# Kernel optimization log

Measured on AMD Instinct MI355X. Metric: run time of the kernel, lower is better.

Reference implementation:

```python
import jax, jax.numpy as jnp
import numpy as np

N_NODES = 100000
N_EDGES = 1280000
D_IN = 64
D_HID = 64


def _sage_conv(x, src, dst, deg, Wl, bl, Wr):
    # gather source-node features per edge, scatter-mean to destination nodes
    msg = x[src]                                            # [E, d]
    agg = jax.ops.segment_sum(msg, dst, num_segments=N_NODES)  # [N, d]
    mean = agg / deg                                        # [N, d]
    # PyG SAGEConv: lin_l(aggregated) + lin_r(root); bias lives in lin_l
    return mean @ Wl.T + bl + x @ Wr.T


def setup_inputs() -> dict:
    key = jax.random.key(0)
    ks = jax.random.split(key, 10)
    x = jax.random.normal(ks[0], (N_NODES, D_IN), dtype=jnp.float32)
    edge_index = jax.random.randint(ks[1], (2, N_EDGES), 0, N_NODES, dtype=jnp.int64)
    s = 1.0 / np.sqrt(D_IN)
    W1l = jax.random.uniform(ks[2], (D_HID, D_IN), jnp.float32, -s, s)
    W1r = jax.random.uniform(ks[3], (D_HID, D_IN), jnp.float32, -s, s)
    b1 = jax.random.uniform(ks[4], (D_HID,), jnp.float32, -s, s)
    s2 = 1.0 / np.sqrt(D_HID)
    W2l = jax.random.uniform(ks[5], (D_HID, D_HID), jnp.float32, -s2, s2)
    W2r = jax.random.uniform(ks[6], (D_HID, D_HID), jnp.float32, -s2, s2)
    b2 = jax.random.uniform(ks[7], (D_HID,), jnp.float32, -s2, s2)
    Wh = jax.random.uniform(ks[8], (1, D_HID), jnp.float32, -s2, s2)
    bh = jax.random.uniform(ks[9], (1,), jnp.float32, -s2, s2)
    return {"x": x, "edge_index": edge_index, "W1l": W1l, "W1r": W1r, "b1": b1,
            "W2l": W2l, "W2r": W2r, "b2": b2, "Wh": Wh, "bh": bh}


def reference(x, edge_index, W1l, W1r, b1, W2l, W2r, b2, Wh, bh):
    src, dst = edge_index[0], edge_index[1]
    # in-degree for mean aggregation (clamped to avoid div-by-zero)
    deg = jax.ops.segment_sum(jnp.ones((N_EDGES,), jnp.float32), dst,
                              num_segments=N_NODES)
    deg = jnp.maximum(deg, 1.0)[:, None]                    # [N, 1]
    h = jax.nn.relu(_sage_conv(x, src, dst, deg, W1l, b1, W1r))
    h = jax.nn.relu(_sage_conv(h, src, dst, deg, W2l, b2, W2r))
    out = (h @ Wh.T + bh)[:, 0]                             # [N]
    return out, h
```

## Files before the change

kernel.cpp:

```cpp
#include <hip/hip_runtime.h>

#define N_NODES 100000
#define N_EDGES 1280000
#define D 64
#define NPAD 102400
#define CAP 48
#define NBUCK 391
#define AB 313
#define NT16 6250
#define XQ (N_NODES * 16)
#define CVTOT (XQ + 32 + 4096)
#define SPLIT 720000
#define CV1 384
#define CV2 384

typedef __attribute__((ext_vector_type(8))) short bf16x8;
typedef __attribute__((ext_vector_type(4))) float f32x4;
typedef __attribute__((ext_vector_type(2))) float f32x2;

__device__ __forceinline__ unsigned short f2bf(float f) {
    union { float f; unsigned u; } c; c.f = f;
    unsigned u = c.u;
    return (unsigned short)((u + 0x7FFF + ((u >> 16) & 1)) >> 16);
}
__device__ __forceinline__ float fp8d(unsigned b) {
    unsigned t = ((b & 0x80u) << 24) | ((b & 0x7fu) << 20);
    union { unsigned u; float f; } c; c.u = t;
    return c.f * 1.32922799578491587e36f;
}
__device__ __forceinline__ unsigned char f2fp8(float f) {
    f = fminf(fmaxf(f, -448.f), 448.f);
    float g = f * 7.52316384526264005e-37f;
    union { float f; unsigned u; } c; c.f = g;
    unsigned gb = c.u;
    unsigned r = (((gb & 0x7fffffffu) + 0x7ffffu + ((gb >> 20) & 1u)) >> 20) & 0x7fu;
    return (unsigned char)(((gb >> 24) & 0x80u) | r);
}

__device__ __forceinline__ void cvt_range(
    int gtid, int gsz, int lo0, int hi,
    const float* __restrict__ x,
    const float* __restrict__ W1l, const float* __restrict__ W1r,
    const float* __restrict__ W2l, const float* __restrict__ W2r,
    unsigned short* __restrict__ xb, unsigned short* __restrict__ h1b,
    unsigned char* __restrict__ x8, unsigned char* __restrict__ h8,
    unsigned short* __restrict__ wb)
{
    for (int i = lo0 + gtid; i < hi; i += gsz) {
        if (i < XQ) {
            float4 v = ((const float4*)x)[i];
            ((ushort4*)xb)[i] = make_ushort4(f2bf(v.x), f2bf(v.y), f2bf(v.z), f2bf(v.w));
            ((uchar4*)x8)[i]  = make_uchar4(f2fp8(v.x), f2fp8(v.y), f2fp8(v.z), f2fp8(v.w));
        } else if (i < XQ + 32) {
            int k = i - XQ;
            if (k < 16) {
                ((ushort4*)xb)[(size_t)N_NODES * 16 + k] = make_ushort4(0,0,0,0);
                ((unsigned*)x8)[(size_t)N_NODES * 16 + k] = 0u;
            } else {
                ((ushort4*)h1b)[(size_t)N_NODES * 16 + (k - 16)] = make_ushort4(0,0,0,0);
                ((unsigned*)h8)[(size_t)N_NODES * 16 + (k - 16)] = 0u;
            }
        } else {
            int wf = i - XQ - 32;
            int m = wf >> 10, k = wf & 1023;
            const float* s = (m == 0) ? W1l : (m == 1) ? W1r : (m == 2) ? W2l : W2r;
            float4 v = ((const float4*)s)[k];
            ((ushort4*)wb)[m * 1024 + k] =
                make_ushort4(f2bf(v.x), f2bf(v.y), f2bf(v.z), f2bf(v.w));
        }
    }
}

__global__ __launch_bounds__(512) void prep_kernel(
    const float* __restrict__ x,
    const int* __restrict__ src, const int* __restrict__ dst,
    const float* __restrict__ W1l, const float* __restrict__ W1r,
    const float* __restrict__ W2l, const float* __restrict__ W2r,
    unsigned short* __restrict__ xb, unsigned short* __restrict__ h1b,
    unsigned char* __restrict__ x8, unsigned char* __restrict__ h8,
    unsigned short* __restrict__ wb,
    int* __restrict__ sorted, int* __restrict__ exclT)
{
    __shared__ int cntA[392];
    __shared__ int excl[392];
    __shared__ int stage_pk[4096];

    const int t   = threadIdx.x;
    const int bid = blockIdx.x;

    if (bid < AB) {
        const int e0 = bid * 4096;
        const int cbatch = min(4096, N_EDGES - e0);

        if (t < 392) cntA[t] = 0;
        __syncthreads();

        int mb[8], mr[8], mpk[8];
#pragma unroll
        for (int i = 0; i < 8; ++i) {
            int idx = i * 512 + t;
            mb[i] = -1;
            if (idx < cbatch) {
                int e = e0 + idx;
                int s = src[e], d = dst[e];
                int b = d >> 8;
                mb[i]  = b;
                mpk[i] = (s << 8) | (d & 255);
                mr[i]  = atomicAdd(&cntA[b], 1);
            }
        }
        __syncthreads();

        if (t < 64) {
            int pre[7], tot = 0;
            if (t < 56) {
#pragma unroll
                for (int i = 0; i < 7; ++i) { pre[i] = tot; tot += cntA[t * 7 + i]; }
            }
            int sc = tot;
#pragma unroll
            for (int off = 1; off < 64; off <<= 1) {
                int u = __shfl_up(sc, off, 64);
                if (t >= off) sc += u;
            }
            int ex = sc - tot;
            if (t < 56) {
#pragma unroll
                for (int i = 0; i < 7; ++i) excl[t * 7 + i] = ex + pre[i];
            }
        }
        __syncthreads();

#pragma unroll
        for (int i = 0; i < 8; ++i) {
            if (mb[i] >= 0)
                stage_pk[excl[mb[i]] + mr[i]] = mpk[i];
        }
        __syncthreads();

#pragma unroll
        for (int i = 0; i < 8; ++i) {
            int idx = i * 512 + t;
            if (idx < cbatch) sorted[e0 + idx] = stage_pk[idx];
        }
        if (t < 392) exclT[bid * 392 + t] = excl[t];
    } else {
        const int gtid = (bid - AB) * 512 + t;
        cvt_range(gtid, CV1 * 512, 0, SPLIT,
                  x, W1l, W1r, W2l, W2r, xb, h1b, x8, h8, wb);
    }
}

__global__ __launch_bounds__(512) void binB_kernel(
    const int* __restrict__ sorted, const int* __restrict__ exclT,
    int* __restrict__ csr, int* __restrict__ deg,
    const float* __restrict__ x,
    const float* __restrict__ W1l, const float* __restrict__ W1r,
    const float* __restrict__ W2l, const float* __restrict__ W2r,
    unsigned short* __restrict__ xb, unsigned short* __restrict__ h1b,
    unsigned char* __restrict__ x8, unsigned char* __restrict__ h8,
    unsigned short* __restrict__ wb)
{
    __shared__ int cur[256];
    __shared__ __align__(16) int lcsr[256 * CAP];

    const int t = threadIdx.x;
    const int k = blockIdx.x;

    if (k < NBUCK) {
        if (t < 256) cur[t] = 0;
        __syncthreads();

        for (int u = t; u < 2 * AB; u += 512) {
            int seg = u >> 1, half = u & 1;
            int s0  = exclT[seg * 392 + k];
            int cnt = exclT[seg * 392 + k + 1] - s0;
            int b0 = half ? (cnt >> 1) : 0;
            int b1 = half ? cnt : (cnt >> 1);
            const int* sp = sorted + seg * 4096 + s0 + b0;
            int m = b1 - b0;
            if (m > 0) {
                int pk = sp[0];
                for (int e = 0; e < m; ++e) {
                    int nxt = (e + 1 < m) ? sp[e + 1] : 0;
                    int nl = pk & 255;
                    int r  = atomicAdd(&cur[nl], 1);
                    if (r < CAP) lcsr[nl * CAP + r] = pk >> 8;
                    pk = nxt;
                }
            }
        }
        __syncthreads();

        const int base = k * 256;
        for (int i = t; i < 4096; i += 512) {
            int r = i >> 4, cc = i & 15;
            if (cc < 12) {
                int lenr = min(cur[r], CAP);
                if (cc * 4 < lenr)
                    *(int4*)(csr + (size_t)(base + r) * CAP + cc * 4) =
                        *(const int4*)(lcsr + r * CAP + cc * 4);
            }
        }
        if (t < 256) deg[base + t] = cur[t];
    } else {
        const int gtid = (k - NBUCK) * 512 + t;
        cvt_range(gtid, CV2 * 512, SPLIT, CVTOT,
                  x, W1l, W1r, W2l, W2r, xb, h1b, x8, h8, wb);
    }
}

template <int LAYER>
__global__ __launch_bounds__(256) void layer_kernel(
    const int* __restrict__ csr, const int* __restrict__ deg_g,
    const unsigned char*  __restrict__ feat8,
    const unsigned short* __restrict__ root_b,
    const unsigned short* __restrict__ wl_b,
    const float* __restrict__ bl,
    const unsigned short* __restrict__ wr_b,
    unsigned short* __restrict__ hout_b,
    unsigned char*  __restrict__ hout8,
    float* __restrict__ hout_f,
    const float* __restrict__ Wh, const float* __restrict__ bh,
    float* __restrict__ out)
{
    __shared__ __align__(16) char lds[9472];
    unsigned short* sA = (unsigned short*)lds;
    unsigned short* sX = sA + 16 * 72;
    float* sH    = (float*)(lds + 4608);
    float* spart = (float*)(lds + 8960);

    const int tid = threadIdx.x;
    const int n0  = blockIdx.x * 16;

    const int jt = tid >> 6;
    const int l64 = tid & 63;
    const int rowl = l64 & 15, quad = l64 >> 4;
    const unsigned short* wlp = wl_b + (jt * 16 + rowl) * 64 + quad * 8;
    const unsigned short* wrp = wr_b + (jt * 16 + rowl) * 64 + quad * 8;
    bf16x8 b0 = *(const bf16x8*)(wlp);
    bf16x8 b1 = *(const bf16x8*)(wlp + 32);
    bf16x8 b2 = *(const bf16x8*)(wrp);
    bf16x8 b3 = *(const bf16x8*)(wrp + 32);
    float bj = bl[jt * 16 + rowl];

    {
        int row = tid >> 4, c4 = tid & 15;
        ushort4 x4 = ((const ushort4*)root_b)[(size_t)(n0 + row) * 16 + c4];
        *(ushort4*)(sX + row * 72 + c4 * 4) = x4;
    }

    {
        const uint2* fb2 = (const uint2*)feat8;
        const int g   = tid >> 4;
        const int l   = tid & 15;
        const int h   = l >> 3;
        const int lo  = l & 7;
        const int n   = n0 + g;
        const int* rp = csr + (size_t)n * CAP;
        const int dg  = deg_g[n];
        const int id0 = rp[l];
        const int len = (dg < CAP) ? dg : CAP;
        f32x2 a0 = {0.f, 0.f}, a1 = {0.f, 0.f}, a2 = {0.f, 0.f}, a3 = {0.f, 0.f};

#if __has_builtin(__builtin_amdgcn_cvt_pk_f32_fp8)
#define GCHUNK(IDEXPR)                                                       \
        {                                                                    \
            int id_ = (IDEXPR);                                              \
            uint2 w[8];                                                      \
            _Pragma("unroll")                                                \
            for (int i = 0; i < 8; ++i)                                      \
                w[i] = fb2[(__shfl(id_, 2 * i + h, 16) << 3) + lo];          \
            _Pragma("unroll")                                                \
            for (int i = 0; i < 8; ++i) {                                    \
                a0 += __builtin_amdgcn_cvt_pk_f32_fp8((int)w[i].x, false);   \
                a1 += __builtin_amdgcn_cvt_pk_f32_fp8((int)w[i].x, true);    \
                a2 += __builtin_amdgcn_cvt_pk_f32_fp8((int)w[i].y, false);   \
                a3 += __builtin_amdgcn_cvt_pk_f32_fp8((int)w[i].y, true);    \
            }                                                                \
        }
#else
#define GCHUNK(IDEXPR)                                                       \
        {                                                                    \
            int id_ = (IDEXPR);                                              \
            uint2 w[8];                                                      \
            _Pragma("unroll")                                                \
            for (int i = 0; i < 8; ++i)                                      \
                w[i] = fb2[(__shfl(id_, 2 * i + h, 16) << 3) + lo];          \
            _Pragma("unroll")                                                \
            for (int i = 0; i < 8; ++i) {                                    \
                f32x2 p0 = {fp8d(w[i].x & 255), fp8d((w[i].x >> 8) & 255)};  \
                f32x2 p1 = {fp8d((w[i].x >> 16) & 255), fp8d(w[i].x >> 24)}; \
                f32x2 p2 = {fp8d(w[i].y & 255), fp8d((w[i].y >> 8) & 255)};  \
                f32x2 p3 = {fp8d((w[i].y >> 16) & 255), fp8d(w[i].y >> 24)}; \
                a0 += p0; a1 += p1; a2 += p2; a3 += p3;                      \
            }                                                                \
        }
#endif

        GCHUNK((l < len) ? id0 : N_NODES);
        for (int cb = 16; cb < len; cb += 16) {
            int idxl = cb + l;
            GCHUNK((idxl < len) ? rp[idxl] : N_NODES);
        }
#undef GCHUNK

        a0.x += __shfl_xor(a0.x, 8); a0.y += __shfl_xor(a0.y, 8);
        a1.x += __shfl_xor(a1.x, 8); a1.y += __shfl_xor(a1.y, 8);
        a2.x += __shfl_xor(a2.x, 8); a2.y += __shfl_xor(a2.y, 8);
        a3.x += __shfl_xor(a3.x, 8); a3.y += __shfl_xor(a3.y, 8);
        float inv = 1.0f / fmaxf((float)dg, 1.0f);
        if (h == 0) {
            *(ushort4*)(sA + g * 72 + lo * 8) =
                make_ushort4(f2bf(a0.x * inv), f2bf(a0.y * inv),
                             f2bf(a1.x * inv), f2bf(a1.y * inv));
            *(ushort4*)(sA + g * 72 + lo * 8 + 4) =
                make_ushort4(f2bf(a2.x * inv), f2bf(a2.y * inv),
                             f2bf(a3.x * inv), f2bf(a3.y * inv));
        }
    }
    __syncthreads();

    const unsigned short* ap = sA + rowl * 72 + quad * 8;
    const unsigned short* xp = sX + rowl * 72 + quad * 8;
    bf16x8 am0 = *(const bf16x8*)(ap);
    bf16x8 am1 = *(const bf16x8*)(ap + 32);
    bf16x8 ax0 = *(const bf16x8*)(xp);
    bf16x8 ax1 = *(const bf16x8*)(xp + 32);

    f32x4 acc = {0.f, 0.f, 0.f, 0.f};
    acc = __builtin_amdgcn_mfma_f32_16x16x32_bf16(am0, b0, acc, 0, 0, 0);
    acc = __builtin_amdgcn_mfma_f32_16x16x32_bf16(am1, b1, acc, 0, 0, 0);
    acc = __builtin_amdgcn_mfma_f32_16x16x32_bf16(ax0, b2, acc, 0, 0, 0);
    acc = __builtin_amdgcn_mfma_f32_16x16x32_bf16(ax1, b3, acc, 0, 0, 0);

#pragma unroll
    for (int r = 0; r < 4; ++r) {
        int node = quad * 4 + r;
        sH[node * 68 + jt * 16 + rowl] = fmaxf(acc[r] + bj, 0.f);
    }
    __syncthreads();

    if (LAYER == 2 && tid < 128) {
        int node = tid >> 3, q = tid & 7;
        float p = 0.f;
#pragma unroll
        for (int c = 0; c < 2; ++c) {
            float4 hv = *(const float4*)(sH + node * 68 + q * 8 + c * 4);
            float4 wv = ((const float4*)Wh)[q * 2 + c];
            p += hv.x * wv.x + hv.y * wv.y + hv.z * wv.z + hv.w * wv.w;
        }
        spart[tid] = p;
    }

    {
        int row = tid >> 4, c4 = tid & 15;
        int n = n0 + row;
        const float* hp = sH + row * 68 + c4 * 4;
        if (LAYER == 1) {
            ((ushort4*)hout_b)[(size_t)n * 16 + c4] =
                make_ushort4(f2bf(hp[0]), f2bf(hp[1]), f2bf(hp[2]), f2bf(hp[3]));
            ((uchar4*)hout8)[(size_t)n * 16 + c4] =
                make_uchar4(f2fp8(hp[0]), f2fp8(hp[1]), f2fp8(hp[2]), f2fp8(hp[3]));
        } else {
            ((float4*)hout_f)[(size_t)n * 16 + c4] =
                make_float4(hp[0], hp[1], hp[2], hp[3]);
        }
    }

    if (LAYER == 2) {
        __syncthreads();
        if (tid < 16) {
            float s = bh[0];
#pragma unroll
            for (int q = 0; q < 8; ++q) s += spart[tid * 8 + q];
            out[n0 + tid] = s;
        }
    }
}

extern "C" void kernel_launch(void* const* d_in, const int* in_sizes, int n_in,
                              void* d_out, int out_size, void* d_ws, size_t ws_size,
                              hipStream_t stream) {
    const float* x   = (const float*)d_in[0];
    const int*   ei  = (const int*)d_in[1];
    const int*   src = ei;
    const int*   dst = ei + N_EDGES;
    const float* W1l = (const float*)d_in[2];
    const float* W1r = (const float*)d_in[3];
    const float* b1  = (const float*)d_in[4];
    const float* W2l = (const float*)d_in[5];
    const float* W2r = (const float*)d_in[6];
    const float* b2  = (const float*)d_in[7];
    const float* Wh  = (const float*)d_in[8];
    const float* bh  = (const float*)d_in[9];

    float* out   = (float*)d_out;
    float* h_out = out + N_NODES;

    int* wsi = (int*)d_ws;
    int* deg = wsi;
    int* csr = deg + NPAD;
    unsigned short* wb  = (unsigned short*)(csr + NBUCK * 256 * CAP);
    unsigned short* x_b = wb + 16384;
    unsigned short* h1b = x_b + (size_t)(N_NODES + 1) * D;
    unsigned char*  x8  = (unsigned char*)(h1b + (size_t)(N_NODES + 1) * D);
    unsigned char*  h8  = x8 + (size_t)(N_NODES + 1) * D;
    int* sorted = (int*)h1b;
    int* exclT  = sorted + AB * 4096;

    unsigned short* w1l_b = wb;
    unsigned short* w1r_b = wb + 4096;
    unsigned short* w2l_b = wb + 8192;
    unsigned short* w2r_b = wb + 12288;

    prep_kernel<<<AB + CV1, 512, 0, stream>>>(
        x, src, dst, W1l, W1r, W2l, W2r, x_b, h1b, x8, h8, wb, sorted, exclT);

    binB_kernel<<<NBUCK + CV2, 512, 0, stream>>>(
        sorted, exclT, csr, deg,
        x, W1l, W1r, W2l, W2r, x_b, h1b, x8, h8, wb);

    layer_kernel<1><<<NT16, 256, 0, stream>>>(
        csr, deg, x8, x_b, w1l_b, b1, w1r_b, h1b, h8, nullptr,
        nullptr, nullptr, nullptr);
    layer_kernel<2><<<NT16, 256, 0, stream>>>(
        csr, deg, h8, h1b, w2l_b, b2, w2r_b, nullptr, nullptr, h_out,
        Wh, bh, out);
}
```

Before: 166.2 us.

## Shrink layer blocks to 8 nodes with 128 threads, two output tiles per wave

```diff
diff --git a/kernel.cpp b/kernel.cpp
--- a/kernel.cpp
+++ b/kernel.cpp
@@ -7,7 +7,7 @@
 #define CAP 48
 #define NBUCK 391
 #define AB 313
-#define NT16 6250
+#define NT8 12500
 #define XQ (N_NODES * 16)
 #define CVTOT (XQ + 32 + 4096)
 #define SPLIT 720000
@@ -211,7 +211,7 @@
 }
 
 template <int LAYER>
-__global__ __launch_bounds__(256) void layer_kernel(
+__global__ __launch_bounds__(128) void layer_kernel(
     const int* __restrict__ csr, const int* __restrict__ deg_g,
     const unsigned char*  __restrict__ feat8,
     const unsigned short* __restrict__ root_b,
@@ -224,25 +224,26 @@
     const float* __restrict__ Wh, const float* __restrict__ bh,
     float* __restrict__ out)
 {
-    __shared__ __align__(16) char lds[9472];
+    __shared__ __align__(16) char lds[4736];
     unsigned short* sA = (unsigned short*)lds;
-    unsigned short* sX = sA + 16 * 72;
-    float* sH    = (float*)(lds + 4608);
-    float* spart = (float*)(lds + 8960);
+    unsigned short* sX = sA + 8 * 72;
+    float* sH    = (float*)(lds + 2304);
+    float* spart = (float*)(lds + 4480);
 
     const int tid = threadIdx.x;
-    const int n0  = blockIdx.x * 16;
-
-    const int jt = tid >> 6;
+    const int n0  = blockIdx.x * 8;
+    const int wv  = tid >> 6;
     const int l64 = tid & 63;
     const int rowl = l64 & 15, quad = l64 >> 4;
-    const unsigned short* wlp = wl_b + (jt * 16 + rowl) * 64 + quad * 8;
-    const unsigned short* wrp = wr_b + (jt * 16 + rowl) * 64 + quad * 8;
-    bf16x8 b0 = *(const bf16x8*)(wlp);
-    bf16x8 b1 = *(const bf16x8*)(wlp + 32);
-    bf16x8 b2 = *(const bf16x8*)(wrp);
-    bf16x8 b3 = *(const bf16x8*)(wrp + 32);
-    float bj = bl[jt * 16 + rowl];
+
+    const int jt0 = wv * 2;
+    const unsigned short* wlp0 = wl_b + (jt0 * 16 + rowl) * 64 + quad * 8;
+    const unsigned short* wrp0 = wr_b + (jt0 * 16 + rowl) * 64 + quad * 8;
+    bf16x8 c00 = *(const bf16x8*)(wlp0);
+    bf16x8 c01 = *(const bf16x8*)(wlp0 + 32);
+    bf16x8 c02 = *(const bf16x8*)(wrp0);
+    bf16x8 c03 = *(const bf16x8*)(wrp0 + 32);
+    float bj0 = bl[jt0 * 16 + rowl];
 
     {
         int row = tid >> 4, c4 = tid & 15;
@@ -321,34 +322,52 @@
     }
     __syncthreads();
 
-    const unsigned short* ap = sA + rowl * 72 + quad * 8;
-    const unsigned short* xp = sX + rowl * 72 + quad * 8;
+    const unsigned short* ap = sA + (rowl & 7) * 72 + quad * 8;
+    const unsigned short* xp = sX + (rowl & 7) * 72 + quad * 8;
     bf16x8 am0 = *(const bf16x8*)(ap);
     bf16x8 am1 = *(const bf16x8*)(ap + 32);
     bf16x8 ax0 = *(const bf16x8*)(xp);
     bf16x8 ax1 = *(const bf16x8*)(xp + 32);
 
-    f32x4 acc = {0.f, 0.f, 0.f, 0.f};
-    acc = __builtin_amdgcn_mfma_f32_16x16x32_bf16(am0, b0, acc, 0, 0, 0);
-    acc = __builtin_amdgcn_mfma_f32_16x16x32_bf16(am1, b1, acc, 0, 0, 0);
-    acc = __builtin_amdgcn_mfma_f32_16x16x32_bf16(ax0, b2, acc, 0, 0, 0);
-    acc = __builtin_amdgcn_mfma_f32_16x16x32_bf16(ax1, b3, acc, 0, 0, 0);
+    const int jt1 = jt0 + 1;
+    const unsigned short* wlp1 = wl_b + (jt1 * 16 + rowl) * 64 + quad * 8;
+    const unsigned short* wrp1 = wr_b + (jt1 * 16 + rowl) * 64 + quad * 8;
+    bf16x8 c10 = *(const bf16x8*)(wlp1);
+    bf16x8 c11 = *(const bf16x8*)(wlp1 + 32);
+    bf16x8 c12 = *(const bf16x8*)(wrp1);
+    bf16x8 c13 = *(const bf16x8*)(wrp1 + 32);
+    float bj1 = bl[jt1 * 16 + rowl];
+
+    f32x4 acc0 = {0.f, 0.f, 0.f, 0.f};
+    acc0 = __builtin_amdgcn_mfma_f32_16x16x32_bf16(am0, c00, acc0, 0, 0, 0);
+    acc0 = __builtin_amdgcn_mfma_f32_16x16x32_bf16(am1, c01, acc0, 0, 0, 0);
+    acc0 = __builtin_amdgcn_mfma_f32_16x16x32_bf16(ax0, c02, acc0, 0, 0, 0);
+    acc0 = __builtin_amdgcn_mfma_f32_16x16x32_bf16(ax1, c03, acc0, 0, 0, 0);
+
+    f32x4 acc1 = {0.f, 0.f, 0.f, 0.f};
+    acc1 = __builtin_amdgcn_mfma_f32_16x16x32_bf16(am0, c10, acc1, 0, 0, 0);
+    acc1 = __builtin_amdgcn_mfma_f32_16x16x32_bf16(am1, c11, acc1, 0, 0, 0);
+    acc1 = __builtin_amdgcn_mfma_f32_16x16x32_bf16(ax0, c12, acc1, 0, 0, 0);
+    acc1 = __builtin_amdgcn_mfma_f32_16x16x32_bf16(ax1, c13, acc1, 0, 0, 0);
 
 #pragma unroll
     for (int r = 0; r < 4; ++r) {
         int node = quad * 4 + r;
-        sH[node * 68 + jt * 16 + rowl] = fmaxf(acc[r] + bj, 0.f);
+        if (node < 8) {
+            sH[node * 68 + jt0 * 16 + rowl] = fmaxf(acc0[r] + bj0, 0.f);
+            sH[node * 68 + jt1 * 16 + rowl] = fmaxf(acc1[r] + bj1, 0.f);
+        }
     }
     __syncthreads();
 
-    if (LAYER == 2 && tid < 128) {
+    if (LAYER == 2 && tid < 64) {
         int node = tid >> 3, q = tid & 7;
         float p = 0.f;
 #pragma unroll
         for (int c = 0; c < 2; ++c) {
             float4 hv = *(const float4*)(sH + node * 68 + q * 8 + c * 4);
-            float4 wv = ((const float4*)Wh)[q * 2 + c];
-            p += hv.x * wv.x + hv.y * wv.y + hv.z * wv.z + hv.w * wv.w;
+            float4 wv2 = ((const float4*)Wh)[q * 2 + c];
+            p += hv.x * wv2.x + hv.y * wv2.y + hv.z * wv2.z + hv.w * wv2.w;
         }
         spart[tid] = p;
     }
@@ -370,7 +389,7 @@
 
     if (LAYER == 2) {
         __syncthreads();
-        if (tid < 16) {
+        if (tid < 8) {
             float s = bh[0];
 #pragma unroll
             for (int q = 0; q < 8; ++q) s += spart[tid * 8 + q];
@@ -421,10 +440,10 @@
         sorted, exclT, csr, deg,
         x, W1l, W1r, W2l, W2r, x_b, h1b, x8, h8, wb);
 
-    layer_kernel<1><<<NT16, 256, 0, stream>>>(
+    layer_kernel<1><<<NT8, 128, 0, stream>>>(
         csr, deg, x8, x_b, w1l_b, b1, w1r_b, h1b, h8, nullptr,
         nullptr, nullptr, nullptr);
-    layer_kernel<2><<<NT16, 256, 0, stream>>>(
+    layer_kernel<2><<<NT8, 128, 0, stream>>>(
         csr, deg, h8, h1b, w2l_b, b2, w2r_b, nullptr, nullptr, h_out,
         Wh, bh, out);
 }
```

New measurement: 188.2 us. 1.13x slower.
